# Kernel tuning notes

Measured on AMD Instinct MI355X. Metric: run time of the kernel, lower is better.

## Reference

```python
import jax, jax.numpy as jnp
import numpy as np

D_K = 64  # per-head key dim, used for 1/sqrt(d_k) scaling


def setup_inputs() -> dict:
    key = jax.random.key(0)
    ks = jax.random.split(key, 9)
    B, S, D, H, DK, DV = 2, 4096, 512, 8, 64, 64
    s = 0.02
    return {
        "x": jax.random.normal(ks[0], (B, S, D), dtype=jnp.float32),
        "Wq": jax.random.normal(ks[1], (H, D, DK), dtype=jnp.float32) * s,
        "bq": jax.random.normal(ks[2], (H, DK), dtype=jnp.float32) * s,
        "Wk": jax.random.normal(ks[3], (H, D, DK), dtype=jnp.float32) * s,
        "bk": jax.random.normal(ks[4], (H, DK), dtype=jnp.float32) * s,
        "Wv": jax.random.normal(ks[5], (H, D, DV), dtype=jnp.float32) * s,
        "bv": jax.random.normal(ks[6], (H, DV), dtype=jnp.float32) * s,
        "Wo": jax.random.normal(ks[7], (H * DV, D), dtype=jnp.float32) * s,
        "bo": jax.random.normal(ks[8], (D,), dtype=jnp.float32) * s,
    }


def reference(x, Wq, bq, Wk, bk, Wv, bv, Wo, bo):
    # Per-head projections, vectorized over heads: [B,H,S,dk/dv]
    q = jnp.einsum("bsd,hdk->bhsk", x, Wq) + bq[None, :, None, :]
    k = jnp.einsum("bsd,hdk->bhsk", x, Wk) + bk[None, :, None, :]
    v = jnp.einsum("bsd,hdv->bhsv", x, Wv) + bv[None, :, None, :]
    # Scaled dot-product attention (no mask; dropout inactive at eval)
    scores = jnp.einsum("bhsk,bhtk->bhst", q, k) / jnp.sqrt(jnp.float32(D_K))
    attn = jax.nn.softmax(scores, axis=-1)
    o = jnp.einsum("bhst,bhtv->bhsv", attn, v)
    # Concat heads along feature dim: [B,S,H*dv]
    B, H, S, DV = o.shape
    concat = jnp.transpose(o, (0, 2, 1, 3)).reshape(B, S, H * DV)
    return concat @ Wo + bo
```

## Files before the change

kernel.cpp:

```cpp
#include <hip/hip_runtime.h>
#include <hip/hip_bf16.h>

typedef __attribute__((ext_vector_type(8))) short bf16x8;
typedef __attribute__((ext_vector_type(4))) float f32x4;
typedef __attribute__((ext_vector_type(16))) float f32x16;
typedef __attribute__((ext_vector_type(4))) unsigned short u16x4;
typedef __attribute__((ext_vector_type(4))) unsigned int u32x4;

#define NB 2
#define NS 4096
#define ND 512
#define NH 8

__device__ __forceinline__ unsigned short f2bf(float f) {
  unsigned int u = __float_as_uint(f);
  u += 0x7fffu + ((u >> 16) & 1u);
  return (unsigned short)(u >> 16);
}

__device__ __forceinline__ float bf2f(unsigned short h) {
  return __uint_as_float(((unsigned)h) << 16);
}

__device__ __forceinline__ float exp2_hw(float x) {
  float r;
  asm("v_exp_f32 %0, %1" : "=v"(r) : "v"(x));
  return r;
}

__device__ __forceinline__ unsigned cvtpk(float lo, float hi) {
  unsigned r;
  asm("v_cvt_pk_bf16_f32 %0, %1, %2" : "=v"(r) : "v"(lo), "v"(hi));
  return r;
}

__device__ __forceinline__ void swap32(unsigned& a, unsigned& b) {
  asm("v_permlane32_swap_b32 %0, %1" : "+v"(a), "+v"(b));
}

__device__ __forceinline__ bf16x8 mkfrag(unsigned w0, unsigned w1,
                                         unsigned w2, unsigned w3) {
  u32x4 u = {w0, w1, w2, w3};
  return __builtin_bit_cast(bf16x8, u);
}

__global__ void pack_kernel(const float* __restrict__ x,
                            const float* __restrict__ Wq,
                            const float* __restrict__ Wk,
                            const float* __restrict__ Wv,
                            const float* __restrict__ Wo,
                            unsigned short* __restrict__ x_bf,
                            unsigned short* __restrict__ w3,
                            unsigned short* __restrict__ wo_t)
{
  int idx = blockIdx.x * 256 + threadIdx.x;
  const int NX4 = NB * NS * ND / 4;
  const int NW = 512 * 512;
  if (idx < NX4) {
    const float4 f = ((const float4*)x)[idx];
    u16x4 o;
    o[0] = f2bf(f.x); o[1] = f2bf(f.y); o[2] = f2bf(f.z); o[3] = f2bf(f.w);
    ((u16x4*)x_bf)[idx] = o;
  } else if (idx < NX4 + 3 * NW) {
    int j = idx - NX4;
    int p = j / NW;
    int r = j - p * NW;
    int n = r >> 9, d = r & 511;
    int h = n >> 6, o = n & 63;
    const float* W = (p == 0) ? Wq : (p == 1) ? Wk : Wv;
    w3[j] = f2bf(W[(h * 512 + d) * 64 + o]);
  } else if (idx < NX4 + 4 * NW) {
    int j = idx - NX4 - 3 * NW;
    int n = j >> 9, kk = j & 511;
    wo_t[j] = f2bf(Wo[kk * 512 + n]);
  }
}

template <int MODE>
__global__ void gemm_bt(const unsigned short* __restrict__ A,
                        const unsigned short* __restrict__ Bm,
                        const float* __restrict__ b0,
                        const float* __restrict__ b1,
                        const float* __restrict__ b2,
                        unsigned short* __restrict__ qo,
                        unsigned short* __restrict__ ko,
                        unsigned short* __restrict__ vo,
                        float* __restrict__ fo) {
  __shared__ unsigned short Al[128 * 32];
  __shared__ unsigned short Bl[128 * 32];
  const int t = threadIdx.x;
  const int m0 = blockIdx.x * 128;
  const int n0 = blockIdx.y * 128;
  const int lane = t & 63;
  const int w = t >> 6;
  const int wm = w >> 1, wn = w & 1;
  const int c = lane & 15, g = lane >> 4;

  f32x4 acc[4][4];
#pragma unroll
  for (int i = 0; i < 4; ++i)
#pragma unroll
    for (int j = 0; j < 4; ++j) acc[i][j] = (f32x4){0.f, 0.f, 0.f, 0.f};

  const int srow = t >> 1, sseg = (t & 1) * 16;
  const unsigned short* Ap = A + (size_t)(m0 + srow) * 512 + sseg;
  const unsigned short* Bp = Bm + (size_t)(n0 + srow) * 512 + sseg;
  unsigned short* Alp = &Al[srow * 32 + sseg];
  unsigned short* Blp = &Bl[srow * 32 + sseg];

  for (int k0 = 0; k0 < 512; k0 += 32) {
    bf16x8 ra0 = *(const bf16x8*)(Ap + k0);
    bf16x8 ra1 = *(const bf16x8*)(Ap + k0 + 8);
    bf16x8 rb0 = *(const bf16x8*)(Bp + k0);
    bf16x8 rb1 = *(const bf16x8*)(Bp + k0 + 8);
    __syncthreads();
    *(bf16x8*)(Alp) = ra0;
    *(bf16x8*)(Alp + 8) = ra1;
    *(bf16x8*)(Blp) = rb0;
    *(bf16x8*)(Blp + 8) = rb1;
    __syncthreads();
    bf16x8 af[4], bfr[4];
#pragma unroll
    for (int mf = 0; mf < 4; ++mf)
      af[mf] = *(const bf16x8*)&Al[(wm * 64 + mf * 16 + c) * 32 + g * 8];
#pragma unroll
    for (int nf = 0; nf < 4; ++nf)
      bfr[nf] = *(const bf16x8*)&Bl[(wn * 64 + nf * 16 + c) * 32 + g * 8];
#pragma unroll
    for (int mf = 0; mf < 4; ++mf)
#pragma unroll
      for (int nf = 0; nf < 4; ++nf)
        acc[mf][nf] = __builtin_amdgcn_mfma_f32_16x16x32_bf16(
            af[mf], bfr[nf], acc[mf][nf], 0, 0, 0);
  }

  if (MODE == 0) {
    const int proj = n0 >> 9;
    const float* bias = proj == 0 ? b0 : (proj == 1 ? b1 : b2);
    unsigned short* dst01 = proj == 0 ? qo : ko;
    const float scale = proj == 0 ? 0.18033688011112042f : 1.0f;
#pragma unroll
    for (int nf = 0; nf < 4; ++nf) {
      const int col5 = (n0 + wn * 64 + nf * 16 + c) & 511;
      const int h = col5 >> 6, o = col5 & 63;
      const float bb = bias[col5];
#pragma unroll
      for (int mf = 0; mf < 4; ++mf) {
#pragma unroll
        for (int r = 0; r < 4; ++r) {
          const int m = m0 + wm * 64 + mf * 16 + g * 4 + r;
          const int b = m >> 12, s = m & 4095;
          const unsigned short hb = f2bf((acc[mf][nf][r] + bb) * scale);
          if (proj < 2)
            dst01[((size_t)((b * NH + h) * NS + s)) * 64 + o] = hb;
          else
            vo[((size_t)((b * NH + h) * 64 + o)) * NS + s] = hb;
        }
      }
    }
  } else {
#pragma unroll
    for (int nf = 0; nf < 4; ++nf) {
      const int col = n0 + wn * 64 + nf * 16 + c;
      const float bb = b0[col];
#pragma unroll
      for (int mf = 0; mf < 4; ++mf) {
#pragma unroll
        for (int r = 0; r < 4; ++r) {
          const int m = m0 + wm * 64 + mf * 16 + g * 4 + r;
          fo[(size_t)m * 512 + col] = acc[mf][nf][r] + bb;
        }
      }
    }
  }
}

template <int SPLITS>
__global__ __launch_bounds__(256, 4) void attn_kernel(
    const unsigned short* __restrict__ q,
    const unsigned short* __restrict__ k,
    const unsigned short* __restrict__ vt,
    unsigned short* __restrict__ cc,
    unsigned short* __restrict__ op,
    float* __restrict__ ml)
{
  union SMemU {
    struct { unsigned short Kl[2][4096]; unsigned short Vl[2][4096]; } kv;
    unsigned short Ol[4][32][68];
  };
  __shared__ SMemU sm;
  const int t = threadIdx.x;
  const int w = t >> 6, lane = t & 63;
  const int col = lane & 31, hi = lane >> 5;
  const int bh = blockIdx.y & 15;
  const int sp = blockIdx.y >> 4;
  const int b = bh >> 3, h = bh & 7;
  const int q0 = blockIdx.x * 128 + w * 32;
  const int kbase = sp * (NS / SPLITS);

  const unsigned short* qh = q + (size_t)bh * NS * 64;
  const unsigned short* kh = k + (size_t)bh * NS * 64;
  const unsigned short* vh = vt + (size_t)bh * 64 * NS;

  bf16x8 qf[4];
#pragma unroll
  for (int c = 0; c < 4; ++c)
    qf[c] = *(const bf16x8*)&qh[(size_t)(q0 + col) * 64 + c * 16 + hi * 8];

  const int r0 = t >> 3, r1 = r0 + 32;
  const int ch = t & 7;
  const int koff0 = r0 * 64 + ((ch ^ (r0 & 7)) << 3);
  const int koff1 = r1 * 64 + ((ch ^ (r1 & 7)) << 3);

  f32x16 ot0, ot1;
#pragma unroll
  for (int r = 0; r < 16; ++r) { ot0[r] = 0.f; ot1[r] = 0.f; }
  float m_ = -1.0e30f, l_ = 0.f;

  {
    bf16x8 a0 = *(const bf16x8*)&kh[(size_t)(kbase + r0) * 64 + ch * 8];
    bf16x8 a1 = *(const bf16x8*)&kh[(size_t)(kbase + r1) * 64 + ch * 8];
    bf16x8 v0 = *(const bf16x8*)&vh[(size_t)r0 * NS + kbase + ch * 8];
    bf16x8 v1 = *(const bf16x8*)&vh[(size_t)r1 * NS + kbase + ch * 8];
    *(bf16x8*)&sm.kv.Kl[0][koff0] = a0;
    *(bf16x8*)&sm.kv.Kl[0][koff1] = a1;
    *(bf16x8*)&sm.kv.Vl[0][koff0] = v0;
    *(bf16x8*)&sm.kv.Vl[0][koff1] = v1;
    __syncthreads();
  }

  const int NT = NS / (64 * SPLITS);
  for (int it = 0; it < NT; ++it) {
    const int cur = it & 1;
    bf16x8 pk0, pk1, pv0, pv1;
    if (it + 1 < NT) {
      const int tn = kbase + (it + 1) * 64;
      pk0 = *(const bf16x8*)&kh[(size_t)(tn + r0) * 64 + ch * 8];
      pk1 = *(const bf16x8*)&kh[(size_t)(tn + r1) * 64 + ch * 8];
      pv0 = *(const bf16x8*)&vh[(size_t)r0 * NS + tn + ch * 8];
      pv1 = *(const bf16x8*)&vh[(size_t)r1 * NS + tn + ch * 8];
    }

    f32x16 p0, p1;
#pragma unroll
    for (int r = 0; r < 16; ++r) { p0[r] = 0.f; p1[r] = 0.f; }
#pragma unroll
    for (int c = 0; c < 4; ++c) {
      const int cidx = (((2 * c + hi) ^ (col & 7)) << 3);
      bf16x8 kf0 = *(const bf16x8*)&sm.kv.Kl[cur][col * 64 + cidx];
      bf16x8 kf1 = *(const bf16x8*)&sm.kv.Kl[cur][(col + 32) * 64 + cidx];
      p0 = __builtin_amdgcn_mfma_f32_32x32x16_bf16(kf0, qf[c], p0, 0, 0, 0);
      p1 = __builtin_amdgcn_mfma_f32_32x32x16_bf16(kf1, qf[c], p1, 0, 0, 0);
    }

    float mx[8];
#pragma unroll
    for (int r = 0; r < 8; ++r)
      mx[r] = fmaxf(fmaxf(p0[r], p0[r + 8]), fmaxf(p1[r], p1[r + 8]));
#pragma unroll
    for (int s = 4; s >= 1; s >>= 1)
#pragma unroll
      for (int r = 0; r < 8; ++r)
        if (r < s) mx[r] = fmaxf(mx[r], mx[r + s]);
    float pm = mx[0];
    pm = fmaxf(pm, __shfl_xor(pm, 32, 64));
    if (__any(pm > m_ + 8.f)) {
      const float resc = exp2_hw(m_ - pm);
      m_ = pm;
      l_ *= resc;
#pragma unroll
      for (int r = 0; r < 16; ++r) { ot0[r] *= resc; ot1[r] *= resc; }
    }
    float e0[16], e1[16];
#pragma unroll
    for (int r = 0; r < 16; ++r) {
      e0[r] = exp2_hw(p0[r] - m_);
      e1[r] = exp2_hw(p1[r] - m_);
    }
    float smv[8];
#pragma unroll
    for (int r = 0; r < 8; ++r)
      smv[r] = (e0[r] + e0[r + 8]) + (e1[r] + e1[r + 8]);
#pragma unroll
    for (int s = 4; s >= 1; s >>= 1)
#pragma unroll
      for (int r = 0; r < 8; ++r)
        if (r < s) smv[r] += smv[r + s];
    float rs = smv[0];
    rs += __shfl_xor(rs, 32, 64);
    l_ += rs;

    unsigned g0[8], g1[8];
#pragma unroll
    for (int gg = 0; gg < 8; ++gg) {
      g0[gg] = cvtpk(e0[2 * gg], e0[2 * gg + 1]);
      g1[gg] = cvtpk(e1[2 * gg], e1[2 * gg + 1]);
    }
    bf16x8 pb[4];
    {
      unsigned a, c2, b2, d2;
      a = g0[0]; b2 = g0[2]; swap32(a, b2);
      c2 = g0[1]; d2 = g0[3]; swap32(c2, d2);
      pb[0] = mkfrag(a, c2, b2, d2);
      a = g0[4]; b2 = g0[6]; swap32(a, b2);
      c2 = g0[5]; d2 = g0[7]; swap32(c2, d2);
      pb[1] = mkfrag(a, c2, b2, d2);
      a = g1[0]; b2 = g1[2]; swap32(a, b2);
      c2 = g1[1]; d2 = g1[3]; swap32(c2, d2);
      pb[2] = mkfrag(a, c2, b2, d2);
      a = g1[4]; b2 = g1[6]; swap32(a, b2);
      c2 = g1[5]; d2 = g1[7]; swap32(c2, d2);
      pb[3] = mkfrag(a, c2, b2, d2);
    }

#pragma unroll
    for (int ks = 0; ks < 4; ++ks) {
      const int cidx = (((2 * ks + hi) ^ (col & 7)) << 3);
      bf16x8 vf0 = *(const bf16x8*)&sm.kv.Vl[cur][col * 64 + cidx];
      bf16x8 vf1 = *(const bf16x8*)&sm.kv.Vl[cur][(col + 32) * 64 + cidx];
      ot0 = __builtin_amdgcn_mfma_f32_32x32x16_bf16(vf0, pb[ks], ot0, 0, 0, 0);
      ot1 = __builtin_amdgcn_mfma_f32_32x32x16_bf16(vf1, pb[ks], ot1, 0, 0, 0);
    }

    if (it + 1 < NT) {
      __syncthreads();
      *(bf16x8*)&sm.kv.Kl[cur ^ 1][koff0] = pk0;
      *(bf16x8*)&sm.kv.Kl[cur ^ 1][koff1] = pk1;
      *(bf16x8*)&sm.kv.Vl[cur ^ 1][koff0] = pv0;
      *(bf16x8*)&sm.kv.Vl[cur ^ 1][koff1] = pv1;
      __syncthreads();
    }
  }

  __syncthreads();

  const float inv = (SPLITS == 1) ? (1.0f / l_) : 1.0f;
#pragma unroll
  for (int r = 0; r < 16; ++r) {
    const int dvb = (r & 3) + 8 * (r >> 2) + 4 * hi;
    sm.Ol[w][col][dvb] = f2bf(ot0[r] * inv);
    sm.Ol[w][col][dvb + 32] = f2bf(ot1[r] * inv);
  }
  if (SPLITS == 2 && hi == 0) {
    float2 mm = {m_, l_};
    *(float2*)&ml[((size_t)(sp * 16 + bh) * NS + q0 + col) * 2] = mm;
  }
  asm volatile("s_waitcnt lgkmcnt(0)" ::: "memory");
  const int row = lane >> 1;
#pragma unroll
  for (int p = 0; p < 4; ++p) {
    const int chunk = (lane & 1) + 2 * p;
    bf16x8 vv = *(const bf16x8*)&sm.Ol[w][row][chunk * 8];
    if (SPLITS == 1)
      *(bf16x8*)&cc[((size_t)(b * NS + q0 + row)) * 512 + h * 64 + chunk * 8] = vv;
    else
      *(bf16x8*)&op[((size_t)(sp * 16 + bh) * NS + q0 + row) * 64 + chunk * 8] = vv;
  }
}

__global__ void combine_kernel(const unsigned short* __restrict__ op,
                               const float* __restrict__ ml,
                               unsigned short* __restrict__ cc) {
  const int id = blockIdx.x * 256 + threadIdx.x;
  const int chunk = id & 7;
  const int qq = (id >> 3) & 4095;
  const int bh = id >> 15;
  const int b = bh >> 3, h = bh & 7;
  const float2 ml0 = *(const float2*)&ml[((size_t)bh * NS + qq) * 2];
  const float2 ml1 = *(const float2*)&ml[((size_t)(16 + bh) * NS + qq) * 2];
  const float m = fmaxf(ml0.x, ml1.x);
  const float w0 = exp2_hw(ml0.x - m), w1 = exp2_hw(ml1.x - m);
  const float invl = 1.0f / (ml0.y * w0 + ml1.y * w1);
  const bf16x8 o0 =
      *(const bf16x8*)&op[((size_t)bh * NS + qq) * 64 + chunk * 8];
  const bf16x8 o1 =
      *(const bf16x8*)&op[((size_t)(16 + bh) * NS + qq) * 64 + chunk * 8];
  bf16x8 out;
#pragma unroll
  for (int j = 0; j < 8; ++j) {
    const float v = (bf2f((unsigned short)o0[j]) * w0 +
                     bf2f((unsigned short)o1[j]) * w1) * invl;
    out[j] = (short)f2bf(v);
  }
  *(bf16x8*)&cc[((size_t)(b * NS + qq)) * 512 + h * 64 + chunk * 8] = out;
}

extern "C" void kernel_launch(void* const* d_in, const int* in_sizes, int n_in,
                              void* d_out, int out_size, void* d_ws, size_t ws_size,
                              hipStream_t stream) {
  const float* x  = (const float*)d_in[0];
  const float* Wq = (const float*)d_in[1];
  const float* bq = (const float*)d_in[2];
  const float* Wk = (const float*)d_in[3];
  const float* bk = (const float*)d_in[4];
  const float* Wv = (const float*)d_in[5];
  const float* bv = (const float*)d_in[6];
  const float* Wo = (const float*)d_in[7];
  const float* bo = (const float*)d_in[8];

  unsigned char* ws = (unsigned char*)d_ws;
  unsigned short* x_bf = (unsigned short*)(ws);
  unsigned short* w3   = (unsigned short*)(ws + 8388608);
  unsigned short* wo_t = (unsigned short*)(ws + 9961472);
  unsigned short* qb   = (unsigned short*)(ws + 10485760);
  unsigned short* kb   = (unsigned short*)(ws + 18874368);
  unsigned short* vb   = (unsigned short*)(ws + 27262976);
  unsigned short* op   = (unsigned short*)(ws + 35651584);
  float*          mlp  = (float*)(ws + 52428800);
  unsigned short* cc   = x_bf;

  const bool two_split = ws_size >= 53477376ull;

  pack_kernel<<<8192, 256, 0, stream>>>(x, Wq, Wk, Wv, Wo, x_bf, w3, wo_t);
  gemm_bt<0><<<dim3(64, 12), 256, 0, stream>>>(x_bf, w3, bq, bk, bv, qb, kb, vb,
                                               nullptr);
  if (two_split) {
    attn_kernel<2><<<dim3(32, 32), 256, 0, stream>>>(qb, kb, vb, nullptr, op,
                                                     mlp);
    combine_kernel<<<2048, 256, 0, stream>>>(op, mlp, cc);
  } else {
    attn_kernel<1><<<dim3(32, 16), 256, 0, stream>>>(qb, kb, vb, cc, nullptr,
                                                     nullptr);
  }
  gemm_bt<1><<<dim3(64, 4), 256, 0, stream>>>(cc, wo_t, bo, nullptr, nullptr,
                                              nullptr, nullptr, nullptr,
                                              (float*)d_out);
}
```

Before: 160.6 us.

## Process two query sets per wave and load K/V with global_load_lds

Each wave now handles 64 queries as two 32-query sets. Every K and V fragment read from shared memory therefore feeds twice as many MFMAs, and the grid is halved. K/V tiles are fetched straight from global memory into LDS with global_load_lds, with the swizzle applied on the source address. This replaces register staging and cuts the barriers to one per iteration. The softmax for the two query sets is interleaved with the PV MFMAs under s_setprio, and launch bounds are lowered to 2 blocks to make room for the larger register footprint, which lowers occupancy.

```diff
diff --git a/kernel.cpp b/kernel.cpp
--- a/kernel.cpp
+++ b/kernel.cpp
@@ -42,6 +42,13 @@
                                          unsigned w2, unsigned w3) {
   u32x4 u = {w0, w1, w2, w3};
   return __builtin_bit_cast(bf16x8, u);
+}
+
+__device__ __forceinline__ void gload_lds16(const unsigned short* g,
+                                            unsigned short* l) {
+  __builtin_amdgcn_global_load_lds(
+      (const __attribute__((address_space(1))) unsigned int*)g,
+      (__attribute__((address_space(3))) unsigned int*)l, 16, 0, 0);
 }
 
 __global__ void pack_kernel(const float* __restrict__ x,
@@ -175,8 +182,59 @@
   }
 }
 
+__device__ __forceinline__ void softmax_qset(f32x16& pA, f32x16& pB,
+                                             float& m_, float& l_,
+                                             f32x16& o0, f32x16& o1,
+                                             bf16x8* pb) {
+  float a[8];
+#pragma unroll
+  for (int r = 0; r < 8; ++r)
+    a[r] = fmaxf(fmaxf(pA[r], pA[r + 8]), fmaxf(pB[r], pB[r + 8]));
+  float pm = fmaxf(fmaxf(fmaxf(a[0], a[1]), fmaxf(a[2], a[3])),
+                   fmaxf(fmaxf(a[4], a[5]), fmaxf(a[6], a[7])));
+  pm = fmaxf(pm, __shfl_xor(pm, 32, 64));
+  if (__any(pm > m_ + 8.f)) {
+    const float resc = exp2_hw(m_ - pm);
+    m_ = pm;
+    l_ *= resc;
+#pragma unroll
+    for (int r = 0; r < 16; ++r) { o0[r] *= resc; o1[r] *= resc; }
+  }
+#pragma unroll
+  for (int r = 0; r < 16; ++r) {
+    pA[r] = exp2_hw(pA[r] - m_);
+    pB[r] = exp2_hw(pB[r] - m_);
+  }
+  float s[8];
+#pragma unroll
+  for (int r = 0; r < 8; ++r)
+    s[r] = (pA[r] + pA[r + 8]) + (pB[r] + pB[r + 8]);
+  float rs = ((s[0] + s[1]) + (s[2] + s[3])) + ((s[4] + s[5]) + (s[6] + s[7]));
+  rs += __shfl_xor(rs, 32, 64);
+  l_ += rs;
+  unsigned g0[8], g1[8];
+#pragma unroll
+  for (int gg = 0; gg < 8; ++gg) {
+    g0[gg] = cvtpk(pA[2 * gg], pA[2 * gg + 1]);
+    g1[gg] = cvtpk(pB[2 * gg], pB[2 * gg + 1]);
+  }
+  unsigned a1, b1, c1, d1;
+  a1 = g0[0]; b1 = g0[2]; swap32(a1, b1);
+  c1 = g0[1]; d1 = g0[3]; swap32(c1, d1);
+  pb[0] = mkfrag(a1, c1, b1, d1);
+  a1 = g0[4]; b1 = g0[6]; swap32(a1, b1);
+  c1 = g0[5]; d1 = g0[7]; swap32(c1, d1);
+  pb[1] = mkfrag(a1, c1, b1, d1);
+  a1 = g1[0]; b1 = g1[2]; swap32(a1, b1);
+  c1 = g1[1]; d1 = g1[3]; swap32(c1, d1);
+  pb[2] = mkfrag(a1, c1, b1, d1);
+  a1 = g1[4]; b1 = g1[6]; swap32(a1, b1);
+  c1 = g1[5]; d1 = g1[7]; swap32(c1, d1);
+  pb[3] = mkfrag(a1, c1, b1, d1);
+}
+
 template <int SPLITS>
-__global__ __launch_bounds__(256, 4) void attn_kernel(
+__global__ __launch_bounds__(256, 2) void attn_kernel(
     const unsigned short* __restrict__ q,
     const unsigned short* __restrict__ k,
     const unsigned short* __restrict__ vt,
@@ -195,166 +253,134 @@
   const int bh = blockIdx.y & 15;
   const int sp = blockIdx.y >> 4;
   const int b = bh >> 3, h = bh & 7;
-  const int q0 = blockIdx.x * 128 + w * 32;
+  const int q0 = blockIdx.x * 256 + w * 64;
   const int kbase = sp * (NS / SPLITS);
 
   const unsigned short* qh = q + (size_t)bh * NS * 64;
   const unsigned short* kh = k + (size_t)bh * NS * 64;
   const unsigned short* vh = vt + (size_t)bh * 64 * NS;
 
-  bf16x8 qf[4];
-#pragma unroll
-  for (int c = 0; c < 4; ++c)
-    qf[c] = *(const bf16x8*)&qh[(size_t)(q0 + col) * 64 + c * 16 + hi * 8];
-
-  const int r0 = t >> 3, r1 = r0 + 32;
-  const int ch = t & 7;
-  const int koff0 = r0 * 64 + ((ch ^ (r0 & 7)) << 3);
-  const int koff1 = r1 * 64 + ((ch ^ (r1 & 7)) << 3);
-
-  f32x16 ot0, ot1;
-#pragma unroll
-  for (int r = 0; r < 16; ++r) { ot0[r] = 0.f; ot1[r] = 0.f; }
-  float m_ = -1.0e30f, l_ = 0.f;
+  bf16x8 qf[2][4];
+#pragma unroll
+  for (int qs = 0; qs < 2; ++qs)
+#pragma unroll
+    for (int c = 0; c < 4; ++c)
+      qf[qs][c] = *(const bf16x8*)&qh[(size_t)(q0 + qs * 32 + col) * 64 +
+                                      c * 16 + hi * 8];
+
+  const int rl = lane >> 3, chn = lane & 7;
+  const int lk = rl * 64 + ((chn ^ (rl & 7)) << 3);
+  const int lv = rl * NS + ((chn ^ (rl & 7)) << 3);
+
+  f32x16 ot[4];
+#pragma unroll
+  for (int i = 0; i < 4; ++i)
+#pragma unroll
+    for (int r = 0; r < 16; ++r) ot[i][r] = 0.f;
+  float m_[2] = {-1.0e30f, -1.0e30f}, l_[2] = {0.f, 0.f};
+
+  const int NT = NS / (64 * SPLITS);
 
   {
-    bf16x8 a0 = *(const bf16x8*)&kh[(size_t)(kbase + r0) * 64 + ch * 8];
-    bf16x8 a1 = *(const bf16x8*)&kh[(size_t)(kbase + r1) * 64 + ch * 8];
-    bf16x8 v0 = *(const bf16x8*)&vh[(size_t)r0 * NS + kbase + ch * 8];
-    bf16x8 v1 = *(const bf16x8*)&vh[(size_t)r1 * NS + kbase + ch * 8];
-    *(bf16x8*)&sm.kv.Kl[0][koff0] = a0;
-    *(bf16x8*)&sm.kv.Kl[0][koff1] = a1;
-    *(bf16x8*)&sm.kv.Vl[0][koff0] = v0;
-    *(bf16x8*)&sm.kv.Vl[0][koff1] = v1;
+    const unsigned short* gk = kh + (size_t)(kbase + w * 16) * 64;
+    const unsigned short* gv = vh + (size_t)(w * 16) * NS + kbase;
+    gload_lds16(gk + lk, &sm.kv.Kl[0][w * 1024]);
+    gload_lds16(gk + lk + 512, &sm.kv.Kl[0][w * 1024 + 512]);
+    gload_lds16(gv + lv, &sm.kv.Vl[0][w * 1024]);
+    gload_lds16(gv + lv + 8 * NS, &sm.kv.Vl[0][w * 1024 + 512]);
     __syncthreads();
   }
 
-  const int NT = NS / (64 * SPLITS);
   for (int it = 0; it < NT; ++it) {
     const int cur = it & 1;
-    bf16x8 pk0, pk1, pv0, pv1;
     if (it + 1 < NT) {
-      const int tn = kbase + (it + 1) * 64;
-      pk0 = *(const bf16x8*)&kh[(size_t)(tn + r0) * 64 + ch * 8];
-      pk1 = *(const bf16x8*)&kh[(size_t)(tn + r1) * 64 + ch * 8];
-      pv0 = *(const bf16x8*)&vh[(size_t)r0 * NS + tn + ch * 8];
-      pv1 = *(const bf16x8*)&vh[(size_t)r1 * NS + tn + ch * 8];
-    }
-
-    f32x16 p0, p1;
-#pragma unroll
-    for (int r = 0; r < 16; ++r) { p0[r] = 0.f; p1[r] = 0.f; }
+      const unsigned short* gk =
+          kh + (size_t)(kbase + (it + 1) * 64 + w * 16) * 64;
+      const unsigned short* gv =
+          vh + (size_t)(w * 16) * NS + kbase + (it + 1) * 64;
+      gload_lds16(gk + lk, &sm.kv.Kl[cur ^ 1][w * 1024]);
+      gload_lds16(gk + lk + 512, &sm.kv.Kl[cur ^ 1][w * 1024 + 512]);
+      gload_lds16(gv + lv, &sm.kv.Vl[cur ^ 1][w * 1024]);
+      gload_lds16(gv + lv + 8 * NS, &sm.kv.Vl[cur ^ 1][w * 1024 + 512]);
+    }
+
+    bf16x8 kfr[2][4];
 #pragma unroll
     for (int c = 0; c < 4; ++c) {
       const int cidx = (((2 * c + hi) ^ (col & 7)) << 3);
-      bf16x8 kf0 = *(const bf16x8*)&sm.kv.Kl[cur][col * 64 + cidx];
-      bf16x8 kf1 = *(const bf16x8*)&sm.kv.Kl[cur][(col + 32) * 64 + cidx];
-      p0 = __builtin_amdgcn_mfma_f32_32x32x16_bf16(kf0, qf[c], p0, 0, 0, 0);
-      p1 = __builtin_amdgcn_mfma_f32_32x32x16_bf16(kf1, qf[c], p1, 0, 0, 0);
-    }
-
-    float mx[8];
-#pragma unroll
-    for (int r = 0; r < 8; ++r)
-      mx[r] = fmaxf(fmaxf(p0[r], p0[r + 8]), fmaxf(p1[r], p1[r + 8]));
-#pragma unroll
-    for (int s = 4; s >= 1; s >>= 1)
-#pragma unroll
-      for (int r = 0; r < 8; ++r)
-        if (r < s) mx[r] = fmaxf(mx[r], mx[r + s]);
-    float pm = mx[0];
-    pm = fmaxf(pm, __shfl_xor(pm, 32, 64));
-    if (__any(pm > m_ + 8.f)) {
-      const float resc = exp2_hw(m_ - pm);
-      m_ = pm;
-      l_ *= resc;
-#pragma unroll
-      for (int r = 0; r < 16; ++r) { ot0[r] *= resc; ot1[r] *= resc; }
-    }
-    float e0[16], e1[16];
-#pragma unroll
-    for (int r = 0; r < 16; ++r) {
-      e0[r] = exp2_hw(p0[r] - m_);
-      e1[r] = exp2_hw(p1[r] - m_);
-    }
-    float smv[8];
-#pragma unroll
-    for (int r = 0; r < 8; ++r)
-      smv[r] = (e0[r] + e0[r + 8]) + (e1[r] + e1[r + 8]);
-#pragma unroll
-    for (int s = 4; s >= 1; s >>= 1)
-#pragma unroll
-      for (int r = 0; r < 8; ++r)
-        if (r < s) smv[r] += smv[r + s];
-    float rs = smv[0];
-    rs += __shfl_xor(rs, 32, 64);
-    l_ += rs;
-
-    unsigned g0[8], g1[8];
-#pragma unroll
-    for (int gg = 0; gg < 8; ++gg) {
-      g0[gg] = cvtpk(e0[2 * gg], e0[2 * gg + 1]);
-      g1[gg] = cvtpk(e1[2 * gg], e1[2 * gg + 1]);
-    }
-    bf16x8 pb[4];
-    {
-      unsigned a, c2, b2, d2;
-      a = g0[0]; b2 = g0[2]; swap32(a, b2);
-      c2 = g0[1]; d2 = g0[3]; swap32(c2, d2);
-      pb[0] = mkfrag(a, c2, b2, d2);
-      a = g0[4]; b2 = g0[6]; swap32(a, b2);
-      c2 = g0[5]; d2 = g0[7]; swap32(c2, d2);
-      pb[1] = mkfrag(a, c2, b2, d2);
-      a = g1[0]; b2 = g1[2]; swap32(a, b2);
-      c2 = g1[1]; d2 = g1[3]; swap32(c2, d2);
-      pb[2] = mkfrag(a, c2, b2, d2);
-      a = g1[4]; b2 = g1[6]; swap32(a, b2);
-      c2 = g1[5]; d2 = g1[7]; swap32(c2, d2);
-      pb[3] = mkfrag(a, c2, b2, d2);
-    }
-
+      kfr[0][c] = *(const bf16x8*)&sm.kv.Kl[cur][col * 64 + cidx];
+      kfr[1][c] = *(const bf16x8*)&sm.kv.Kl[cur][(col + 32) * 64 + cidx];
+    }
+    f32x16 p0, p1, p2, p3;
+#pragma unroll
+    for (int r = 0; r < 16; ++r) { p0[r] = 0.f; p1[r] = 0.f; p2[r] = 0.f; p3[r] = 0.f; }
+    __builtin_amdgcn_s_setprio(1);
+#pragma unroll
+    for (int c = 0; c < 4; ++c) {
+      p0 = __builtin_amdgcn_mfma_f32_32x32x16_bf16(kfr[0][c], qf[0][c], p0, 0, 0, 0);
+      p1 = __builtin_amdgcn_mfma_f32_32x32x16_bf16(kfr[1][c], qf[0][c], p1, 0, 0, 0);
+      p2 = __builtin_amdgcn_mfma_f32_32x32x16_bf16(kfr[0][c], qf[1][c], p2, 0, 0, 0);
+      p3 = __builtin_amdgcn_mfma_f32_32x32x16_bf16(kfr[1][c], qf[1][c], p3, 0, 0, 0);
+    }
+    __builtin_amdgcn_s_setprio(0);
+
+    bf16x8 vfr[2][4];
 #pragma unroll
     for (int ks = 0; ks < 4; ++ks) {
       const int cidx = (((2 * ks + hi) ^ (col & 7)) << 3);
-      bf16x8 vf0 = *(const bf16x8*)&sm.kv.Vl[cur][col * 64 + cidx];
-      bf16x8 vf1 = *(const bf16x8*)&sm.kv.Vl[cur][(col + 32) * 64 + cidx];
-      ot0 = __builtin_amdgcn_mfma_f32_32x32x16_bf16(vf0, pb[ks], ot0, 0, 0, 0);
-      ot1 = __builtin_amdgcn_mfma_f32_32x32x16_bf16(vf1, pb[ks], ot1, 0, 0, 0);
-    }
-
-    if (it + 1 < NT) {
-      __syncthreads();
-      *(bf16x8*)&sm.kv.Kl[cur ^ 1][koff0] = pk0;
-      *(bf16x8*)&sm.kv.Kl[cur ^ 1][koff1] = pk1;
-      *(bf16x8*)&sm.kv.Vl[cur ^ 1][koff0] = pv0;
-      *(bf16x8*)&sm.kv.Vl[cur ^ 1][koff1] = pv1;
-      __syncthreads();
-    }
-  }
-
-  __syncthreads();
-
-  const float inv = (SPLITS == 1) ? (1.0f / l_) : 1.0f;
-#pragma unroll
-  for (int r = 0; r < 16; ++r) {
-    const int dvb = (r & 3) + 8 * (r >> 2) + 4 * hi;
-    sm.Ol[w][col][dvb] = f2bf(ot0[r] * inv);
-    sm.Ol[w][col][dvb + 32] = f2bf(ot1[r] * inv);
-  }
-  if (SPLITS == 2 && hi == 0) {
-    float2 mm = {m_, l_};
-    *(float2*)&ml[((size_t)(sp * 16 + bh) * NS + q0 + col) * 2] = mm;
-  }
-  asm volatile("s_waitcnt lgkmcnt(0)" ::: "memory");
-  const int row = lane >> 1;
-#pragma unroll
-  for (int p = 0; p < 4; ++p) {
-    const int chunk = (lane & 1) + 2 * p;
-    bf16x8 vv = *(const bf16x8*)&sm.Ol[w][row][chunk * 8];
-    if (SPLITS == 1)
-      *(bf16x8*)&cc[((size_t)(b * NS + q0 + row)) * 512 + h * 64 + chunk * 8] = vv;
-    else
-      *(bf16x8*)&op[((size_t)(sp * 16 + bh) * NS + q0 + row) * 64 + chunk * 8] = vv;
+      vfr[0][ks] = *(const bf16x8*)&sm.kv.Vl[cur][col * 64 + cidx];
+      vfr[1][ks] = *(const bf16x8*)&sm.kv.Vl[cur][(col + 32) * 64 + cidx];
+    }
+
+    bf16x8 pb[4];
+    softmax_qset(p0, p1, m_[0], l_[0], ot[0], ot[1], pb);
+    __builtin_amdgcn_s_setprio(1);
+#pragma unroll
+    for (int ks = 0; ks < 4; ++ks) {
+      ot[0] = __builtin_amdgcn_mfma_f32_32x32x16_bf16(vfr[0][ks], pb[ks], ot[0], 0, 0, 0);
+      ot[1] = __builtin_amdgcn_mfma_f32_32x32x16_bf16(vfr[1][ks], pb[ks], ot[1], 0, 0, 0);
+    }
+    __builtin_amdgcn_s_setprio(0);
+
+    softmax_qset(p2, p3, m_[1], l_[1], ot[2], ot[3], pb);
+    __builtin_amdgcn_s_setprio(1);
+#pragma unroll
+    for (int ks = 0; ks < 4; ++ks) {
+      ot[2] = __builtin_amdgcn_mfma_f32_32x32x16_bf16(vfr[0][ks], pb[ks], ot[2], 0, 0, 0);
+      ot[3] = __builtin_amdgcn_mfma_f32_32x32x16_bf16(vfr[1][ks], pb[ks], ot[3], 0, 0, 0);
+    }
+    __builtin_amdgcn_s_setprio(0);
+
+    __syncthreads();
+  }
+
+#pragma unroll
+  for (int qs = 0; qs < 2; ++qs) {
+    const float inv = (SPLITS == 1) ? (1.0f / l_[qs]) : 1.0f;
+#pragma unroll
+    for (int r = 0; r < 16; ++r) {
+      const int dvb = (r & 3) + 8 * (r >> 2) + 4 * hi;
+      sm.Ol[w][col][dvb] = f2bf(ot[qs * 2][r] * inv);
+      sm.Ol[w][col][dvb + 32] = f2bf(ot[qs * 2 + 1][r] * inv);
+    }
+    if (SPLITS == 2 && hi == 0) {
+      float2 mm = {m_[qs], l_[qs]};
+      *(float2*)&ml[((size_t)(sp * 16 + bh) * NS + q0 + qs * 32 + col) * 2] = mm;
+    }
+    asm volatile("s_waitcnt lgkmcnt(0)" ::: "memory");
+    const int row = lane >> 1;
+#pragma unroll
+    for (int p = 0; p < 4; ++p) {
+      const int chunk = (lane & 1) + 2 * p;
+      bf16x8 vv = *(const bf16x8*)&sm.Ol[w][row][chunk * 8];
+      if (SPLITS == 1)
+        *(bf16x8*)&cc[((size_t)(b * NS + q0 + qs * 32 + row)) * 512 + h * 64 +
+                      chunk * 8] = vv;
+      else
+        *(bf16x8*)&op[((size_t)(sp * 16 + bh) * NS + q0 + qs * 32 + row) * 64 +
+                      chunk * 8] = vv;
+    }
+    asm volatile("s_waitcnt lgkmcnt(0)" ::: "memory");
   }
 }
 
@@ -415,11 +441,11 @@
   gemm_bt<0><<<dim3(64, 12), 256, 0, stream>>>(x_bf, w3, bq, bk, bv, qb, kb, vb,
                                                nullptr);
   if (two_split) {
-    attn_kernel<2><<<dim3(32, 32), 256, 0, stream>>>(qb, kb, vb, nullptr, op,
+    attn_kernel<2><<<dim3(16, 32), 256, 0, stream>>>(qb, kb, vb, nullptr, op,
                                                      mlp);
     combine_kernel<<<2048, 256, 0, stream>>>(op, mlp, cc);
   } else {
-    attn_kernel<1><<<dim3(32, 16), 256, 0, stream>>>(qb, kb, vb, cc, nullptr,
+    attn_kernel<1><<<dim3(16, 16), 256, 0, stream>>>(qb, kb, vb, cc, nullptr,
                                                      nullptr);
   }
   gemm_bt<1><<<dim3(64, 4), 256, 0, stream>>>(cc, wo_t, bo, nullptr, nullptr,
```

Measured after the change: 153.9 us. -4.1%, faster.
